# Performance work log

Hardware: AMD Instinct MI355X
Metric: run time of the kernel (lower is better)

Reference implementation:

```python
import jax, jax.numpy as jnp
import numpy as np

B, S, D_IN, D_OUT = 8, 4096, 1024, 1024
R_F, R_M, R_S = 8, 32, 64
R_TOT = R_F + R_M + R_S  # 104
HID = 64
ALPHA = 1.0


def setup_inputs() -> dict:
    key = jax.random.key(0)
    ks = jax.random.split(key, 10)
    inp = {
        "x": jax.random.normal(ks[0], (B, S, D_IN), dtype=jnp.float32),
        # fresh memory state after reset_memory(): zeros of shape [batch, r_*]
        "mem_fast": jnp.zeros((B, R_F), dtype=jnp.float32),
        "mem_medium": jnp.zeros((B, R_M), dtype=jnp.float32),
        "mem_slow": jnp.zeros((B, R_S), dtype=jnp.float32),
        # frozen base nn.Linear
        "base_w": jax.random.normal(ks[1], (D_OUT, D_IN), dtype=jnp.float32) / np.sqrt(D_IN),
        "base_b": jax.random.normal(ks[2], (D_OUT,), dtype=jnp.float32) * 0.01,
        # LoRA projections: proj_down kaiming-ish, proj_up zero-init per _init_weights
        "pd_w": jax.random.normal(ks[3], (R_TOT, D_IN), dtype=jnp.float32) / np.sqrt(D_IN),
        "pu_w": jax.random.normal(ks[4], (D_OUT, R_TOT), dtype=jnp.float32) * 0.01,
        # gate_net: Linear(D_IN, HID) -> GELU -> Linear(HID, 3) -> Softmax
        "g1_w": jax.random.normal(ks[5], (HID, D_IN), dtype=jnp.float32) / np.sqrt(D_IN),
        "g1_b": jnp.zeros((HID,), dtype=jnp.float32),
        "g2_w": jax.random.normal(ks[6], (3, HID), dtype=jnp.float32) / np.sqrt(HID),
        "g2_b": jnp.zeros((3,), dtype=jnp.float32),
    }
    return inp


def reference(x, mem_fast, mem_medium, mem_slow, base_w, base_b,
              pd_w, pu_w, g1_w, g1_b, g2_w, g2_b):
    # base linear: [B,S,D_out]
    base_out = jnp.einsum("bsd,od->bso", x, base_w) + base_b
    # down projection: [B,S,R_TOT]
    proj = jnp.einsum("bsd,rd->bsr", x, pd_w)
    # per-timescale multiplicative modulation by recurrent memory state
    # (split -> (1+mem)*proj -> concat) == concat memories once
    mem = jnp.concatenate([mem_fast, mem_medium, mem_slow], axis=-1)  # [B,R_TOT]
    modulated = proj * (1.0 + mem[:, None, :])
    # gate_net: Linear -> GELU(exact) -> Linear -> softmax over 3 timescales
    h = jax.nn.gelu(jnp.einsum("bsd,hd->bsh", x, g1_w) + g1_b, approximate=False)
    gates = jax.nn.softmax(jnp.einsum("bsh,gh->bsg", h, g2_w) + g2_b, axis=-1)
    gate_scale = jnp.mean(gates, axis=-1, keepdims=True)  # [B,S,1]
    # up projection and residual combine
    lora_out = jnp.einsum("bsr,or->bso", modulated, pu_w)
    output = base_out + ALPHA * lora_out * gate_scale
    return output
```

## Files before the change

### kernel.cpp

```cpp
#include <hip/hip_runtime.h>
#include <stdint.h>


typedef unsigned short ushort_t;
typedef unsigned short us8 __attribute__((ext_vector_type(8)));
typedef short short8 __attribute__((ext_vector_type(8)));
typedef float f32x4 __attribute__((ext_vector_type(4)));

__device__ __forceinline__ ushort_t f2b(float f) {
  union { float f; uint32_t i; } v; v.f = f;
  uint32_t lsb = (v.i >> 16) & 1u;
  v.i += 0x7fffu + lsb;
  return (ushort_t)(v.i >> 16);
}

__device__ __forceinline__ void async16(const void* g, void* l) {
  __builtin_amdgcn_global_load_lds(
      (const __attribute__((address_space(1))) void*)g,
      (__attribute__((address_space(3))) void*)l, 16, 0, 0);
}

__global__ __launch_bounds__(256) void convert_x(const float* __restrict__ x,
                                                 ushort_t* __restrict__ xb) {
  const size_t i = ((size_t)blockIdx.x * 256 + threadIdx.x) * 8;
  f32x4 a = *(const f32x4*)(x + i);
  f32x4 b = *(const f32x4*)(x + i + 4);
  us8 o;
#pragma unroll
  for (int j = 0; j < 4; j++) { o[j] = f2b(a[j]); o[4 + j] = f2b(b[j]); }
  *(us8*)(xb + i) = o;
}

__global__ void prep_flags(const uint32_t* __restrict__ mf,
                           const uint32_t* __restrict__ mm,
                           const uint32_t* __restrict__ ms,
                           int* __restrict__ flags) {
  int t = threadIdx.x;
  if (t < 8) {
    int f = 0;
    for (int r = 0; r < 8; r++)  f |= ((mf[t * 8 + r]  & 0x7fffffffu) != 0);
    for (int r = 0; r < 32; r++) f |= ((mm[t * 32 + r] & 0x7fffffffu) != 0);
    for (int r = 0; r < 64; r++) f |= ((ms[t * 64 + r] & 0x7fffffffu) != 0);
    flags[t] = f;
  }
}

__global__ __launch_bounds__(128) void prep_w0(const float* __restrict__ base_w,
                                               const float* __restrict__ pu_w,
                                               const float* __restrict__ pd_w,
                                               ushort_t* __restrict__ W0) {
  const int o = blockIdx.x, t = threadIdx.x;
  __shared__ float spu[104];
  if (t < 104) spu[t] = pu_w[o * 104 + t] * (1.0f / 3.0f);
  __syncthreads();
  const int d0 = t * 8;
  float acc[8];
  f32x4 b0 = *(const f32x4*)(base_w + o * 1024 + d0);
  f32x4 b1 = *(const f32x4*)(base_w + o * 1024 + d0 + 4);
#pragma unroll
  for (int j = 0; j < 4; j++) { acc[j] = b0[j]; acc[4 + j] = b1[j]; }
  for (int r = 0; r < 104; r++) {
    f32x4 p0 = *(const f32x4*)(pd_w + r * 1024 + d0);
    f32x4 p1 = *(const f32x4*)(pd_w + r * 1024 + d0 + 4);
    float s = spu[r];
#pragma unroll
    for (int j = 0; j < 4; j++) { acc[j] += s * p0[j]; acc[4 + j] += s * p1[j]; }
  }
  us8 ov;
#pragma unroll
  for (int j = 0; j < 8; j++) ov[j] = f2b(acc[j]);
  *(us8*)(W0 + o * 1024 + d0) = ov;
}

__global__ __launch_bounds__(128) void prep_delta(const float* __restrict__ base_w,
                                                  const float* __restrict__ pu_w,
                                                  const float* __restrict__ pd_w,
                                                  const float* __restrict__ mf,
                                                  const float* __restrict__ mm,
                                                  const float* __restrict__ ms,
                                                  const int* __restrict__ flags,
                                                  ushort_t* __restrict__ Weff) {
  const int o = blockIdx.x, b = blockIdx.y;
  if (flags[b] == 0) return;
  const int t = threadIdx.x;
  __shared__ float spu[104];
  if (t < 104) {
    float mv = (t < 8) ? mf[b * 8 + t]
             : (t < 40) ? mm[b * 32 + (t - 8)]
                        : ms[b * 64 + (t - 40)];
    spu[t] = pu_w[o * 104 + t] * (1.0f + mv) * (1.0f / 3.0f);
  }
  __syncthreads();
  const int d0 = t * 8;
  float acc[8];
  f32x4 b0 = *(const f32x4*)(base_w + o * 1024 + d0);
  f32x4 b1 = *(const f32x4*)(base_w + o * 1024 + d0 + 4);
#pragma unroll
  for (int j = 0; j < 4; j++) { acc[j] = b0[j]; acc[4 + j] = b1[j]; }
  for (int r = 0; r < 104; r++) {
    f32x4 p0 = *(const f32x4*)(pd_w + r * 1024 + d0);
    f32x4 p1 = *(const f32x4*)(pd_w + r * 1024 + d0 + 4);
    float s = spu[r];
#pragma unroll
    for (int j = 0; j < 4; j++) { acc[j] += s * p0[j]; acc[4 + j] += s * p1[j]; }
  }
  us8 ov;
#pragma unroll
  for (int j = 0; j < 8; j++) ov[j] = f2b(acc[j]);
  *(us8*)(Weff + ((size_t)b << 20) + o * 1024 + d0) = ov;
}

__global__ __launch_bounds__(256) void gemm_bt(const ushort_t* __restrict__ xb,
                                               const float* __restrict__ base_b,
                                               const ushort_t* __restrict__ W0,
                                               const ushort_t* __restrict__ Weff,
                                               const int* __restrict__ flags,
                                               float* __restrict__ out) {
  const int bn = blockIdx.x, bm = blockIdx.y, b = blockIdx.z;
  const ushort_t* W = flags[b] ? (Weff + ((size_t)b << 20)) : W0;

  __shared__ __align__(16) short As[128 * 32];
  __shared__ __align__(16) short Bs[128 * 32];

  const int t = threadIdx.x;
  const int wave = t >> 6, lane = t & 63;
  const int row16 = lane & 15, quad = lane >> 4;
  const int wm = (wave >> 1) * 64, wn = (wave & 1) * 64;

  const ushort_t* gA = xb + (((size_t)b * 4096 + bm * 128 + (t >> 2)) << 10) + (t & 3) * 8;
  const ushort_t* gB = W + (((size_t)(bn * 128 + (t >> 2))) << 10) + (t & 3) * 8;
  char* lA = (char*)As + wave * 1024;
  char* lB = (char*)Bs + wave * 1024;

  f32x4 acc[4][4] = {};

  for (int k0 = 0; k0 < 1024; k0 += 32) {
    async16(gA + k0, lA);
    async16(gA + k0 + (64 << 10), lA + 4096);
    async16(gB + k0, lB);
    async16(gB + k0 + (64 << 10), lB + 4096);
    __syncthreads();

    short8 af[4], bf[4];
#pragma unroll
    for (int mi = 0; mi < 4; mi++)
      af[mi] = *(const short8*)(As + (wm + mi * 16 + row16) * 32 + quad * 8);
#pragma unroll
    for (int ni = 0; ni < 4; ni++)
      bf[ni] = *(const short8*)(Bs + (wn + ni * 16 + row16) * 32 + quad * 8);
#pragma unroll
    for (int mi = 0; mi < 4; mi++)
#pragma unroll
      for (int ni = 0; ni < 4; ni++)
        acc[mi][ni] = __builtin_amdgcn_mfma_f32_16x16x32_bf16(af[mi], bf[ni],
                                                              acc[mi][ni], 0, 0, 0);
    __syncthreads();
  }

#pragma unroll
  for (int ni = 0; ni < 4; ni++) {
    const int col = bn * 128 + wn + ni * 16 + row16;
    const float bb = base_b[col];
#pragma unroll
    for (int mi = 0; mi < 4; mi++) {
      const int row = bm * 128 + wm + mi * 16 + quad * 4;
#pragma unroll
      for (int i = 0; i < 4; i++) {
        out[(((size_t)b * 4096 + row + i) << 10) + col] = acc[mi][ni][i] + bb;
      }
    }
  }
}

extern "C" void kernel_launch(void* const* d_in, const int* in_sizes, int n_in,
                              void* d_out, int out_size, void* d_ws, size_t ws_size,
                              hipStream_t stream) {
  const float* x  = (const float*)d_in[0];
  const float* mf = (const float*)d_in[1];
  const float* mm = (const float*)d_in[2];
  const float* ms = (const float*)d_in[3];
  const float* base_w = (const float*)d_in[4];
  const float* base_b = (const float*)d_in[5];
  const float* pd_w = (const float*)d_in[6];
  const float* pu_w = (const float*)d_in[7];

  char* ws = (char*)d_ws;
  int* flags     = (int*)ws;
  ushort_t* W0   = (ushort_t*)(ws + 4096);
  ushort_t* xb   = (ushort_t*)(ws + 4096 + (2u << 20));
  ushort_t* Weff = (ushort_t*)(ws + 4096 + (2u << 20) + (64u << 20));

  prep_flags<<<1, 64, 0, stream>>>((const uint32_t*)mf, (const uint32_t*)mm,
                                   (const uint32_t*)ms, flags);
  convert_x<<<16384, 256, 0, stream>>>(x, xb);
  prep_w0<<<1024, 128, 0, stream>>>(base_w, pu_w, pd_w, W0);
  prep_delta<<<dim3(1024, 8), 128, 0, stream>>>(base_w, pu_w, pd_w, mf, mm, ms,
                                                flags, Weff);
  gemm_bt<<<dim3(8, 32, 8), 256, 0, stream>>>(xb, base_b, W0, Weff, flags,
                                              (float*)d_out);
}
```

Baseline: 366.1 us.

## Fuse weight prep kernels and remap GEMM and convert grids for XCD locality

Folds the flag check, the shared W0 build and the per-batch effective-weight build into one prep kernel that computes its flag per block, which removes two launches and the serial flag dependency. The GEMM moves to a flat 1D grid whose low bits pick the batch and whose tiles are grouped in 8x8 blocks, so tiles sharing inputs are more likely to land on the same XCD and reuse L2. convert_x gets the same batch-interleaved block ordering. The fused prep writes the flags array only from the o==0 block, relying on kernel ordering before the GEMM reads it.

Result: faster. 349.7 us (-4.5%).

```diff
diff --git a/kernel.cpp b/kernel.cpp
--- a/kernel.cpp
+++ b/kernel.cpp
@@ -22,37 +22,54 @@
 
 __global__ __launch_bounds__(256) void convert_x(const float* __restrict__ x,
                                                  ushort_t* __restrict__ xb) {
-  const size_t i = ((size_t)blockIdx.x * 256 + threadIdx.x) * 8;
-  f32x4 a = *(const f32x4*)(x + i);
-  f32x4 b = *(const f32x4*)(x + i + 4);
+  const int flat = blockIdx.x;
+  const int b = flat & 7;
+  const int c = flat >> 3;
+  const size_t i = (((size_t)b * 2048 + c) * 256 + threadIdx.x) * 8;
+  f32x4 a0 = *(const f32x4*)(x + i);
+  f32x4 a1 = *(const f32x4*)(x + i + 4);
   us8 o;
 #pragma unroll
-  for (int j = 0; j < 4; j++) { o[j] = f2b(a[j]); o[4 + j] = f2b(b[j]); }
+  for (int j = 0; j < 4; j++) { o[j] = f2b(a0[j]); o[4 + j] = f2b(a1[j]); }
   *(us8*)(xb + i) = o;
 }
 
-__global__ void prep_flags(const uint32_t* __restrict__ mf,
-                           const uint32_t* __restrict__ mm,
-                           const uint32_t* __restrict__ ms,
-                           int* __restrict__ flags) {
-  int t = threadIdx.x;
-  if (t < 8) {
-    int f = 0;
-    for (int r = 0; r < 8; r++)  f |= ((mf[t * 8 + r]  & 0x7fffffffu) != 0);
-    for (int r = 0; r < 32; r++) f |= ((mm[t * 32 + r] & 0x7fffffffu) != 0);
-    for (int r = 0; r < 64; r++) f |= ((ms[t * 64 + r] & 0x7fffffffu) != 0);
-    flags[t] = f;
+__global__ __launch_bounds__(128) void prep(const float* __restrict__ base_w,
+                                            const float* __restrict__ pu_w,
+                                            const float* __restrict__ pd_w,
+                                            const float* __restrict__ mf,
+                                            const float* __restrict__ mm,
+                                            const float* __restrict__ ms,
+                                            ushort_t* __restrict__ W0,
+                                            ushort_t* __restrict__ Weff,
+                                            int* __restrict__ flags) {
+  const int o = blockIdx.x, y = blockIdx.y, t = threadIdx.x;
+  __shared__ float spu[104];
+  __shared__ int sflag;
+  ushort_t* dst;
+
+  if (y == 0) {
+    if (t < 104) spu[t] = pu_w[o * 104 + t] * (1.0f / 3.0f);
+    dst = W0 + o * 1024;
+    __syncthreads();
+  } else {
+    const int b = y - 1;
+    if (t == 0) sflag = 0;
+    __syncthreads();
+    float mv = 0.0f;
+    if (t < 104) {
+      mv = (t < 8) ? mf[b * 8 + t]
+         : (t < 40) ? mm[b * 32 + (t - 8)]
+                    : ms[b * 64 + (t - 40)];
+      if (mv != 0.0f) sflag = 1;
+      spu[t] = pu_w[o * 104 + t] * (1.0f + mv) * (1.0f / 3.0f);
+    }
+    __syncthreads();
+    if (o == 0 && t == 0) flags[b] = sflag;
+    if (!sflag) return;
+    dst = Weff + ((size_t)b << 20) + o * 1024;
   }
-}
 
-__global__ __launch_bounds__(128) void prep_w0(const float* __restrict__ base_w,
-                                               const float* __restrict__ pu_w,
-                                               const float* __restrict__ pd_w,
-                                               ushort_t* __restrict__ W0) {
-  const int o = blockIdx.x, t = threadIdx.x;
-  __shared__ float spu[104];
-  if (t < 104) spu[t] = pu_w[o * 104 + t] * (1.0f / 3.0f);
-  __syncthreads();
   const int d0 = t * 8;
   float acc[8];
   f32x4 b0 = *(const f32x4*)(base_w + o * 1024 + d0);
@@ -69,45 +86,7 @@
   us8 ov;
 #pragma unroll
   for (int j = 0; j < 8; j++) ov[j] = f2b(acc[j]);
-  *(us8*)(W0 + o * 1024 + d0) = ov;
-}
-
-__global__ __launch_bounds__(128) void prep_delta(const float* __restrict__ base_w,
-                                                  const float* __restrict__ pu_w,
-                                                  const float* __restrict__ pd_w,
-                                                  const float* __restrict__ mf,
-                                                  const float* __restrict__ mm,
-                                                  const float* __restrict__ ms,
-                                                  const int* __restrict__ flags,
-                                                  ushort_t* __restrict__ Weff) {
-  const int o = blockIdx.x, b = blockIdx.y;
-  if (flags[b] == 0) return;
-  const int t = threadIdx.x;
-  __shared__ float spu[104];
-  if (t < 104) {
-    float mv = (t < 8) ? mf[b * 8 + t]
-             : (t < 40) ? mm[b * 32 + (t - 8)]
-                        : ms[b * 64 + (t - 40)];
-    spu[t] = pu_w[o * 104 + t] * (1.0f + mv) * (1.0f / 3.0f);
-  }
-  __syncthreads();
-  const int d0 = t * 8;
-  float acc[8];
-  f32x4 b0 = *(const f32x4*)(base_w + o * 1024 + d0);
-  f32x4 b1 = *(const f32x4*)(base_w + o * 1024 + d0 + 4);
-#pragma unroll
-  for (int j = 0; j < 4; j++) { acc[j] = b0[j]; acc[4 + j] = b1[j]; }
-  for (int r = 0; r < 104; r++) {
-    f32x4 p0 = *(const f32x4*)(pd_w + r * 1024 + d0);
-    f32x4 p1 = *(const f32x4*)(pd_w + r * 1024 + d0 + 4);
-    float s = spu[r];
-#pragma unroll
-    for (int j = 0; j < 4; j++) { acc[j] += s * p0[j]; acc[4 + j] += s * p1[j]; }
-  }
-  us8 ov;
-#pragma unroll
-  for (int j = 0; j < 8; j++) ov[j] = f2b(acc[j]);
-  *(us8*)(Weff + ((size_t)b << 20) + o * 1024 + d0) = ov;
+  *(us8*)(dst + d0) = ov;
 }
 
 __global__ __launch_bounds__(256) void gemm_bt(const ushort_t* __restrict__ xb,
@@ -116,7 +95,14 @@
                                                const ushort_t* __restrict__ Weff,
                                                const int* __restrict__ flags,
                                                float* __restrict__ out) {
-  const int bn = blockIdx.x, bm = blockIdx.y, b = blockIdx.z;
+  const int flat = blockIdx.x;
+  const int b  = flat & 7;
+  const int i  = flat >> 3;
+  const int g  = i >> 6;
+  const int r  = i & 63;
+  const int bn = r >> 3;
+  const int bm = g * 8 + (r & 7);
+
   const ushort_t* W = flags[b] ? (Weff + ((size_t)b << 20)) : W0;
 
   __shared__ __align__(16) short As[128 * 32];
@@ -165,8 +151,8 @@
     for (int mi = 0; mi < 4; mi++) {
       const int row = bm * 128 + wm + mi * 16 + quad * 4;
 #pragma unroll
-      for (int i = 0; i < 4; i++) {
-        out[(((size_t)b * 4096 + row + i) << 10) + col] = acc[mi][ni][i] + bb;
+      for (int i2 = 0; i2 < 4; i2++) {
+        out[(((size_t)b * 4096 + row + i2) << 10) + col] = acc[mi][ni][i2] + bb;
       }
     }
   }
@@ -190,12 +176,8 @@
   ushort_t* xb   = (ushort_t*)(ws + 4096 + (2u << 20));
   ushort_t* Weff = (ushort_t*)(ws + 4096 + (2u << 20) + (64u << 20));
 
-  prep_flags<<<1, 64, 0, stream>>>((const uint32_t*)mf, (const uint32_t*)mm,
-                                   (const uint32_t*)ms, flags);
+  prep<<<dim3(1024, 9), 128, 0, stream>>>(base_w, pu_w, pd_w, mf, mm, ms,
+                                          W0, Weff, flags);
   convert_x<<<16384, 256, 0, stream>>>(x, xb);
-  prep_w0<<<1024, 128, 0, stream>>>(base_w, pu_w, pd_w, W0);
-  prep_delta<<<dim3(1024, 8), 128, 0, stream>>>(base_w, pu_w, pd_w, mf, mm, ms,
-                                                flags, Weff);
-  gemm_bt<<<dim3(8, 32, 8), 256, 0, stream>>>(xb, base_b, W0, Weff, flags,
-                                              (float*)d_out);
+  gemm_bt<<<2048, 256, 0, stream>>>(xb, base_b, W0, Weff, flags, (float*)d_out);
 }
```
